# Optimization experiments

Hardware: AMD Instinct MI355X
Metric: run time of the kernel (lower is better)

## Reference

```python
import jax, jax.numpy as jnp
import numpy as np

S, B, D, H, WIN, L = 8192, 4, 512, 8, 64, 6
HD = D // H
EPS = 1e-5


def setup_inputs() -> dict:
    key = jax.random.key(0)
    ks = jax.random.split(key, 6)
    s = 0.02
    return {
        "src": jax.random.normal(ks[0], (S, B, D), jnp.float32),
        "Wqkv": jax.random.normal(ks[1], (L, 3 * D, D), jnp.float32) * s,
        "bqkv": jnp.zeros((L, 3 * D), jnp.float32),
        "Wo": jax.random.normal(ks[2], (L, D, D), jnp.float32) * s,
        "bo": jnp.zeros((L, D), jnp.float32),
        "W1": jax.random.normal(ks[3], (L, 4 * D, D), jnp.float32) * s,
        "bf1": jnp.zeros((L, 4 * D), jnp.float32),
        "W2": jax.random.normal(ks[4], (L, D, 4 * D), jnp.float32) * s,
        "bf2": jnp.zeros((L, D), jnp.float32),
        "g1": jnp.ones((L, D), jnp.float32),
        "beta1": jnp.zeros((L, D), jnp.float32),
        "g2": jnp.ones((L, D), jnp.float32),
        "beta2": jnp.zeros((L, D), jnp.float32),
    }


def layernorm(x, g, b):
    m = jnp.mean(x, axis=-1, keepdims=True)
    v = jnp.mean(jnp.square(x - m), axis=-1, keepdims=True)
    return (x - m) * jax.lax.rsqrt(v + EPS) * g + b


def _forward(src, Wqkv, bqkv, Wo, bo, W1, bf1, W2, bf2, g1, beta1, g2, beta2):
    NW = S // WIN
    scale = 1.0 / np.sqrt(HD)
    x = src
    for l in range(L):
        qkv = x @ Wqkv[l].T + bqkv[l]                      # (S,B,3D)
        q, k, v = jnp.split(qkv, 3, axis=-1)
        win = lambda t: t.reshape(NW, WIN, B, H, HD)       # (NW,W,B,H,hd)
        q = win(q) * scale
        k = win(k)
        v = win(v)
        att = jax.nn.softmax(jnp.einsum('nqbhd,nkbhd->nbhqk', q, k), axis=-1)
        o = jnp.einsum('nbhqk,nkbhd->nqbhd', att, v).reshape(S, B, D)
        o = o @ Wo[l].T + bo[l]
        x = layernorm(x + o, g1[l], beta1[l])
        # FFN with ReLU (hidden = 4*d_model)
        f = jax.nn.relu(x @ W1[l].T + bf1[l]) @ W2[l].T + bf2[l]
        x = layernorm(x + f, g2[l], beta2[l])
    return x


def reference(src, Wqkv, bqkv, Wo, bo, W1, bf1, W2, bf2, g1, beta1, g2, beta2):
    return _forward(src, Wqkv, bqkv, Wo, bo, W1, bf1, W2, bf2, g1, beta1, g2, beta2)
```

## Files before the change

kernel.cpp:

```cpp
#include <hip/hip_runtime.h>
#include <hip/hip_bf16.h>

typedef __bf16 bf16x8 __attribute__((ext_vector_type(8)));
typedef float f32x4 __attribute__((ext_vector_type(4)));

static constexpr int NT = 32768;
static constexpr int D_ = 512;
static constexpr int D3 = 1536;
static constexpr int DF = 2048;
static constexpr int L_ = 6;

#define AS1 __attribute__((address_space(1)))
#define AS3 __attribute__((address_space(3)))

__device__ __forceinline__ void gload_lds16(const void* g, void* l) {
  __builtin_amdgcn_global_load_lds((const AS1 void*)g, (AS3 void*)l, 16, 0, 0);
}

template<int K, int NTN, bool RELU>
__global__ __launch_bounds__(256, 4) void gemm128g(
    const __hip_bfloat16* __restrict__ A,
    const __hip_bfloat16* __restrict__ Wp,
    const float* __restrict__ bias,
    __hip_bfloat16* __restrict__ Cout) {
  __shared__ __align__(16) char lds[32768];
  const int t = threadIdx.x;
  const int l = t & 63, w = t >> 6;
  const int lrow = l & 15, lhi = l >> 4;
  const int wr = w >> 1, wc = w & 1;

  const int lin = blockIdx.x;
  const int wg = (lin & 7) * ((int)gridDim.x >> 3) + (lin >> 3);
  const int tm0 = (wg / NTN) * 128, tn0 = (wg % NTN) * 128;

  constexpr int NKT = K / 64;
  constexpr int N = NTN * 128;

  const int srow = t >> 3;
  const int sun = t & 7;
  const int u8 = (sun ^ (srow & 7)) << 3;
  const __hip_bfloat16* sA = A + (size_t)(tm0 + srow) * K + u8;
  const __hip_bfloat16* sA2 = sA + (size_t)64 * K;

  const char* bpB = (const char*)(Wp + (size_t)((tn0 >> 6) + wc) * NKT * 4096) +
                    l * 16;

  const int lo = lrow * 128;
  const int x0 = (lhi ^ (lrow & 7)) << 4;
  const int x1 = ((4 + lhi) ^ (lrow & 7)) << 4;
  const char* pA[2][2];
  pA[0][0] = lds + wr * 8192 + lo + x0;
  pA[0][1] = lds + wr * 8192 + lo + x1;
  pA[1][0] = lds + 16384 + wr * 8192 + lo + x0;
  pA[1][1] = lds + 16384 + wr * 8192 + lo + x1;

  auto stageA = [&](int p, int kt) {
    char* d0 = lds + p * 16384 + w * 1024;
    const __hip_bfloat16* s0 = sA + kt * 64;
    gload_lds16(s0, d0);
    gload_lds16(s0 + (size_t)32 * K, d0 + 4096);
    char* d1 = lds + p * 16384 + 8192 + w * 1024;
    const __hip_bfloat16* s1 = sA2 + kt * 64;
    gload_lds16(s1, d1);
    gload_lds16(s1 + (size_t)32 * K, d1 + 4096);
  };

  f32x4 acc[4][4] = {};
  bf16x8 af[4][2], bf[2][2];

  stageA(0, 0);
  asm volatile("s_waitcnt vmcnt(0)" ::: "memory");
  __builtin_amdgcn_sched_barrier(0);
  __builtin_amdgcn_s_barrier();

  for (int kt = 0; kt < NKT; ++kt) {
    const int p = kt & 1;
    const bool more = (kt + 1 < NKT);
    if (more) stageA(p ^ 1, kt + 1);
    __builtin_amdgcn_sched_barrier(0);
#pragma unroll
    for (int m = 0; m < 4; ++m)
#pragma unroll
      for (int ks = 0; ks < 2; ++ks)
        af[m][ks] = *(const bf16x8*)(pA[p][ks] + m * 2048);
    const char* qb = bpB + (size_t)kt * 8192;
#pragma unroll
    for (int nh = 0; nh < 2; ++nh) {
#pragma unroll
      for (int n = 0; n < 2; ++n)
#pragma unroll
        for (int ks = 0; ks < 2; ++ks)
          bf[n][ks] = *(const bf16x8*)(qb + nh * 4096 + (n * 2 + ks) * 1024);
#pragma unroll
      for (int m = 0; m < 4; ++m)
#pragma unroll
        for (int n = 0; n < 2; ++n)
#pragma unroll
          for (int ks = 0; ks < 2; ++ks)
            acc[m][nh * 2 + n] = __builtin_amdgcn_mfma_f32_16x16x32_bf16(
                af[m][ks], bf[n][ks], acc[m][nh * 2 + n], 0, 0, 0);
    }
    asm volatile("s_waitcnt lgkmcnt(0)" ::: "memory");
    __builtin_amdgcn_sched_barrier(0);
    __builtin_amdgcn_s_barrier();
  }

  char* ep = lds + w * 8192;
#pragma unroll
  for (int n = 0; n < 4; ++n) {
    float bv = bias[tn0 + wc * 64 + n * 16 + lrow];
#pragma unroll
    for (int m = 0; m < 4; ++m)
#pragma unroll
      for (int j = 0; j < 4; ++j) {
        float v = acc[m][n][j] + bv;
        if (RELU) v = fmaxf(v, 0.f);
        int row = m * 16 + lhi * 4 + j;
        int col = n * 16 + lrow;
        *(__hip_bfloat16*)(ep + row * 128 + (((col >> 3) ^ (row & 7)) << 4) +
                           (col & 7) * 2) = __float2bfloat16(v);
      }
  }
  __builtin_amdgcn_sched_barrier(0);
  const int er = l >> 3, ec = l & 7;
#pragma unroll
  for (int p = 0; p < 8; ++p) {
    int r = p * 8 + er;
    uint4 vv = *(const uint4*)(ep + r * 128 + ((ec ^ (r & 7)) << 4));
    *(uint4*)&Cout[(size_t)(tm0 + wr * 64 + r) * N + tn0 + wc * 64 + ec * 8] = vv;
  }
}

__global__ __launch_bounds__(128) void attn_win(
    const __hip_bfloat16* __restrict__ qkv, __hip_bfloat16* __restrict__ o) {
  __shared__ __align__(16) char lds[2 * 18432];
  const int t = threadIdx.x, l = t & 63, w = t >> 6;
  char* vt = lds + w * 18432;
  char* pl = vt + 9216;
  const int wid = blockIdx.x * 2 + w;
  const int h = wid & 7, b = (wid >> 3) & 3, nw = wid >> 5;
  const int lrow = l & 15, lhi = l >> 4;
  const __hip_bfloat16* qp = qkv + (size_t)(nw * 256 + b) * 1536 + h * 64;
  const __hip_bfloat16* kp = qp + 512;
  const __hip_bfloat16* vp = qp + 1024;

  {
    const int d0 = (l & 7) * 8;
    const int r0 = l >> 3;
#pragma unroll
    for (int i = 0; i < 8; ++i) {
      int r = r0 + i * 8;
      union { uint4 u; __hip_bfloat16 e[8]; } vv;
      vv.u = *(const uint4*)(vp + (size_t)r * 6144 + d0);
#pragma unroll
      for (int j = 0; j < 8; ++j)
        *(__hip_bfloat16*)(vt + ((d0 + j) * 72 + r) * 2) = vv.e[j];
    }
  }

  bf16x8 qf[4][2], kf[4][2];
#pragma unroll
  for (int mi = 0; mi < 4; ++mi)
#pragma unroll
    for (int ks = 0; ks < 2; ++ks) {
      int r = mi * 16 + lrow;
      int d = ks * 32 + lhi * 8;
      qf[mi][ks] = __builtin_bit_cast(bf16x8, *(const uint4*)(qp + (size_t)r * 6144 + d));
      kf[mi][ks] = __builtin_bit_cast(bf16x8, *(const uint4*)(kp + (size_t)r * 6144 + d));
    }

  f32x4 s[4][4] = {};
#pragma unroll
  for (int mi = 0; mi < 4; ++mi)
#pragma unroll
    for (int ni = 0; ni < 4; ++ni) {
      s[mi][ni] = __builtin_amdgcn_mfma_f32_16x16x32_bf16(qf[mi][0], kf[ni][0], s[mi][ni], 0, 0, 0);
      s[mi][ni] = __builtin_amdgcn_mfma_f32_16x16x32_bf16(qf[mi][1], kf[ni][1], s[mi][ni], 0, 0, 0);
    }

#pragma unroll
  for (int mi = 0; mi < 4; ++mi)
#pragma unroll
    for (int j = 0; j < 4; ++j) {
      float mx = s[mi][0][j];
#pragma unroll
      for (int ni = 1; ni < 4; ++ni) mx = fmaxf(mx, s[mi][ni][j]);
      mx = fmaxf(mx, __shfl_xor(mx, 1));
      mx = fmaxf(mx, __shfl_xor(mx, 2));
      mx = fmaxf(mx, __shfl_xor(mx, 4));
      mx = fmaxf(mx, __shfl_xor(mx, 8));
      float p[4], sum = 0.f;
#pragma unroll
      for (int ni = 0; ni < 4; ++ni) { p[ni] = __expf(s[mi][ni][j] - mx); sum += p[ni]; }
      sum += __shfl_xor(sum, 1);
      sum += __shfl_xor(sum, 2);
      sum += __shfl_xor(sum, 4);
      sum += __shfl_xor(sum, 8);
      float inv = 1.f / sum;
      int row = mi * 16 + lhi * 4 + j;
#pragma unroll
      for (int ni = 0; ni < 4; ++ni)
        *(__hip_bfloat16*)(pl + (row * 72 + ni * 16 + lrow) * 2) =
            __float2bfloat16(p[ni] * inv);
    }

  bf16x8 pf[4][2], vf[4][2];
#pragma unroll
  for (int mi = 0; mi < 4; ++mi)
#pragma unroll
    for (int ks = 0; ks < 2; ++ks)
      pf[mi][ks] = *(const bf16x8*)(pl + ((mi * 16 + lrow) * 72 + ks * 32 + lhi * 8) * 2);
#pragma unroll
  for (int ni = 0; ni < 4; ++ni)
#pragma unroll
    for (int ks = 0; ks < 2; ++ks)
      vf[ni][ks] = *(const bf16x8*)(vt + ((ni * 16 + lrow) * 72 + ks * 32 + lhi * 8) * 2);

  f32x4 acc[4][4] = {};
#pragma unroll
  for (int mi = 0; mi < 4; ++mi)
#pragma unroll
    for (int ni = 0; ni < 4; ++ni) {
      acc[mi][ni] = __builtin_amdgcn_mfma_f32_16x16x32_bf16(pf[mi][0], vf[ni][0], acc[mi][ni], 0, 0, 0);
      acc[mi][ni] = __builtin_amdgcn_mfma_f32_16x16x32_bf16(pf[mi][1], vf[ni][1], acc[mi][ni], 0, 0, 0);
    }

  __hip_bfloat16* op = o + (size_t)(nw * 256 + b) * 512 + h * 64;
#pragma unroll
  for (int mi = 0; mi < 4; ++mi)
#pragma unroll
    for (int ni = 0; ni < 4; ++ni) {
      int col = ni * 16 + lrow;
#pragma unroll
      for (int j = 0; j < 4; ++j) {
        int row = mi * 16 + lhi * 4 + j;
        op[(size_t)row * 2048 + col] = __float2bfloat16(acc[mi][ni][j]);
      }
    }
}

template<bool LAST>
__global__ __launch_bounds__(256) void ln_res_b(
    __hip_bfloat16* __restrict__ xb, const __hip_bfloat16* __restrict__ f,
    const float* __restrict__ g, const float* __restrict__ be,
    float* __restrict__ xout) {
  const int w = threadIdx.x >> 6, l = threadIdx.x & 63;
  const size_t row = (size_t)blockIdx.x * 4 + w;
  const int c = l * 8;
  union { uint4 u; __hip_bfloat16 e[8]; } xa, fa;
  xa.u = *(const uint4*)(xb + row * 512 + c);
  fa.u = *(const uint4*)(f + row * 512 + c);
  float v[8];
#pragma unroll
  for (int j = 0; j < 8; ++j)
    v[j] = __bfloat162float(xa.e[j]) + __bfloat162float(fa.e[j]);
  float sum = 0.f, sq = 0.f;
#pragma unroll
  for (int j = 0; j < 8; ++j) { sum += v[j]; sq += v[j] * v[j]; }
#pragma unroll
  for (int m = 1; m < 64; m <<= 1) {
    sum += __shfl_xor(sum, m);
    sq += __shfl_xor(sq, m);
  }
  float mean = sum * (1.f / 512.f);
  float var = sq * (1.f / 512.f) - mean * mean;
  float rs = rsqrtf(var + 1e-5f);
  float4 g0 = *(const float4*)(g + c);
  float4 g1v = *(const float4*)(g + c + 4);
  float4 e0 = *(const float4*)(be + c);
  float4 e1 = *(const float4*)(be + c + 4);
  float gg[8] = {g0.x, g0.y, g0.z, g0.w, g1v.x, g1v.y, g1v.z, g1v.w};
  float ee[8] = {e0.x, e0.y, e0.z, e0.w, e1.x, e1.y, e1.z, e1.w};
  float y[8];
  union { uint4 u; __hip_bfloat16 e[8]; } hb;
#pragma unroll
  for (int j = 0; j < 8; ++j) {
    y[j] = (v[j] - mean) * rs * gg[j] + ee[j];
    hb.e[j] = __float2bfloat16(y[j]);
  }
  *(uint4*)(xb + row * 512 + c) = hb.u;
  if (LAST) {
    float4 o0 = {y[0], y[1], y[2], y[3]};
    float4 o1 = {y[4], y[5], y[6], y[7]};
    *(float4*)(xout + row * 512 + c) = o0;
    *(float4*)(xout + row * 512 + c + 4) = o1;
  }
}

__global__ void convw(const float* __restrict__ s, __hip_bfloat16* __restrict__ o) {
  int i = blockIdx.x * 256 + threadIdx.x;
  float4 v = ((const float4*)s)[i];
  __hip_bfloat16 hb[4] = {__float2bfloat16(v.x), __float2bfloat16(v.y),
                          __float2bfloat16(v.z), __float2bfloat16(v.w)};
  ((uint2*)o)[i] = *(uint2*)hb;
}

template<int K, int Nw, bool SCALEQ>
__global__ void convs(const float* __restrict__ s, __hip_bfloat16* __restrict__ o) {
  int i = blockIdx.x * 256 + threadIdx.x;
  int e = i * 4;
  int layer = e / (Nw * K);
  int rem = e - layer * (Nw * K);
  int r = rem / K, c = rem - r * K;
  float4 v = ((const float4*)s)[i];
  float sc = (SCALEQ && r < 512) ? 0.125f : 1.f;
  int didx = layer * (Nw * K) + ((r >> 6) * (K >> 6) + (c >> 6)) * 4096 +
             (((r >> 4) & 3) * 2 + ((c >> 5) & 1)) * 512 + ((c >> 3) & 3) * 128 +
             (r & 15) * 8 + (c & 7);
  __hip_bfloat16 hb[4] = {__float2bfloat16(v.x * sc), __float2bfloat16(v.y * sc),
                          __float2bfloat16(v.z * sc), __float2bfloat16(v.w * sc)};
  *(uint2*)(o + didx) = *(uint2*)hb;
}

__global__ void scaleb(const float* __restrict__ b, float* __restrict__ o) {
  int i = blockIdx.x * 256 + threadIdx.x;
  o[i] = b[i] * (((i % 1536) < 512) ? 0.125f : 1.f);
}

extern "C" void kernel_launch(void* const* d_in, const int* in_sizes, int n_in,
                              void* d_out, int out_size, void* d_ws, size_t ws_size,
                              hipStream_t stream) {
  const float* src  = (const float*)d_in[0];
  const float* Wqkv = (const float*)d_in[1];
  const float* bqkv = (const float*)d_in[2];
  const float* Wo   = (const float*)d_in[3];
  const float* bo   = (const float*)d_in[4];
  const float* W1   = (const float*)d_in[5];
  const float* bf1  = (const float*)d_in[6];
  const float* W2   = (const float*)d_in[7];
  const float* bf2  = (const float*)d_in[8];
  const float* g1   = (const float*)d_in[9];
  const float* be1  = (const float*)d_in[10];
  const float* g2   = (const float*)d_in[11];
  const float* be2  = (const float*)d_in[12];
  float* xout = (float*)d_out;

  char* ws = (char*)d_ws;
  size_t off = 0;
  auto alloc = [&](size_t bytes) {
    char* p = ws + off;
    off += (bytes + 255) & ~(size_t)255;
    return p;
  };

  const size_t wq_b = (size_t)L_ * D3 * D_ * 2;
  const size_t wo_b = (size_t)L_ * D_ * D_ * 2;
  const size_t w1_b = (size_t)L_ * DF * D_ * 2;
  const size_t w2_b = (size_t)L_ * D_ * DF * 2;
  const size_t xb_b = (size_t)NT * 512 * 2;
  auto al = [](size_t v) { return (v + 255) & ~(size_t)255; };
  const size_t persist =
      al(wq_b) + al(wo_b) + al(w1_b) + al(w2_b) + al(L_ * D3 * 4) + al(xb_b);

  int CT = NT;
  while (CT > 2048 && persist + (size_t)CT * 5120 + 65536 > ws_size) CT >>= 1;

  __hip_bfloat16* wqkvb = (__hip_bfloat16*)alloc(wq_b);
  __hip_bfloat16* wob   = (__hip_bfloat16*)alloc(wo_b);
  __hip_bfloat16* w1b   = (__hip_bfloat16*)alloc(w1_b);
  __hip_bfloat16* w2b   = (__hip_bfloat16*)alloc(w2_b);
  float*          bqs   = (float*)alloc((size_t)L_ * D3 * 4);
  __hip_bfloat16* xb    = (__hip_bfloat16*)alloc(xb_b);
  __hip_bfloat16* R     = (__hip_bfloat16*)alloc((size_t)CT * 2048 * 2);
  __hip_bfloat16* OB    = (__hip_bfloat16*)alloc((size_t)CT * 512 * 2);

  convw<<<NT * 512 / 4 / 256, 256, 0, stream>>>(src, xb);
  convs<512, 1536, true><<<L_ * D3 * D_ / 4 / 256, 256, 0, stream>>>(Wqkv, wqkvb);
  convs<512, 512, false><<<L_ * D_ * D_ / 4 / 256, 256, 0, stream>>>(Wo, wob);
  convs<512, 2048, false><<<L_ * DF * D_ / 4 / 256, 256, 0, stream>>>(W1, w1b);
  convs<2048, 512, false><<<L_ * D_ * DF / 4 / 256, 256, 0, stream>>>(W2, w2b);
  scaleb<<<L_ * D3 / 256, 256, 0, stream>>>(bqkv, bqs);

  const int nch = NT / CT;
  for (int c = 0; c < nch; ++c) {
    __hip_bfloat16* xm = xb + (size_t)c * CT * 512;
    float* xo = xout + (size_t)c * CT * 512;
    for (int l = 0; l < L_; ++l) {
      gemm128g<512, 12, false><<<(CT / 128) * 12, 256, 0, stream>>>(
          xm, wqkvb + (size_t)l * D3 * D_, bqs + l * D3, R);
      attn_win<<<CT / 16, 128, 0, stream>>>(R, OB);
      gemm128g<512, 4, false><<<(CT / 128) * 4, 256, 0, stream>>>(
          OB, wob + (size_t)l * D_ * D_, bo + l * D_, R);
      ln_res_b<false><<<CT / 4, 256, 0, stream>>>(xm, R, g1 + l * D_,
                                                  be1 + l * D_, xo);
      gemm128g<512, 16, true><<<(CT / 128) * 16, 256, 0, stream>>>(
          xm, w1b + (size_t)l * DF * D_, bf1 + l * DF, R);
      gemm128g<2048, 4, false><<<(CT / 128) * 4, 256, 0, stream>>>(
          R, w2b + (size_t)l * D_ * DF, bf2 + l * D_, OB);
      if (l == L_ - 1)
        ln_res_b<true><<<CT / 4, 256, 0, stream>>>(xm, OB, g2 + l * D_,
                                                   be2 + l * D_, xo);
      else
        ln_res_b<false><<<CT / 4, 256, 0, stream>>>(xm, OB, g2 + l * D_,
                                                    be2 + l * D_, xo);
    }
  }
}
```

Baseline: 2.226 ms.

## Stage two K-tiles per barrier phase in GEMM with larger LDS buffers

The GEMM kernel now loads two 64-wide K tiles of A into LDS per pipeline phase, using a 64KB double buffer, and computes both before one barrier. This halves the number of workgroup barriers and waits per K sweep and gives the next stage's loads more time to arrive. In exchange LDS per block doubles and launch bounds drop from 4 to 2 blocks per CU, which lowers occupancy and latency hiding across blocks. An explicit vmcnt wait is added before the barrier.

```diff
diff --git a/kernel.cpp b/kernel.cpp
--- a/kernel.cpp
+++ b/kernel.cpp
@@ -18,12 +18,12 @@
 }
 
 template<int K, int NTN, bool RELU>
-__global__ __launch_bounds__(256, 4) void gemm128g(
+__global__ __launch_bounds__(256, 2) void gemm2(
     const __hip_bfloat16* __restrict__ A,
     const __hip_bfloat16* __restrict__ Wp,
     const float* __restrict__ bias,
     __hip_bfloat16* __restrict__ Cout) {
-  __shared__ __align__(16) char lds[32768];
+  __shared__ __align__(16) char lds[65536];
   const int t = threadIdx.x;
   const int l = t & 63, w = t >> 6;
   const int lrow = l & 15, lhi = l >> 4;
@@ -34,6 +34,7 @@
   const int tm0 = (wg / NTN) * 128, tn0 = (wg % NTN) * 128;
 
   constexpr int NKT = K / 64;
+  constexpr int NP = NKT / 2;
   constexpr int N = NTN * 128;
 
   const int srow = t >> 3;
@@ -48,58 +49,65 @@
   const int lo = lrow * 128;
   const int x0 = (lhi ^ (lrow & 7)) << 4;
   const int x1 = ((4 + lhi) ^ (lrow & 7)) << 4;
-  const char* pA[2][2];
-  pA[0][0] = lds + wr * 8192 + lo + x0;
-  pA[0][1] = lds + wr * 8192 + lo + x1;
-  pA[1][0] = lds + 16384 + wr * 8192 + lo + x0;
-  pA[1][1] = lds + 16384 + wr * 8192 + lo + x1;
-
-  auto stageA = [&](int p, int kt) {
-    char* d0 = lds + p * 16384 + w * 1024;
-    const __hip_bfloat16* s0 = sA + kt * 64;
-    gload_lds16(s0, d0);
-    gload_lds16(s0 + (size_t)32 * K, d0 + 4096);
-    char* d1 = lds + p * 16384 + 8192 + w * 1024;
-    const __hip_bfloat16* s1 = sA2 + kt * 64;
-    gload_lds16(s1, d1);
-    gload_lds16(s1 + (size_t)32 * K, d1 + 4096);
+  const char* pbase = lds + wr * 8192 + lo;
+
+  auto stage = [&](int p, int ktb) {
+    char* base = lds + p * 32768 + w * 1024;
+#pragma unroll
+    for (int sub = 0; sub < 2; ++sub) {
+      const int kt = ktb + sub;
+      char* d = base + sub * 16384;
+      const __hip_bfloat16* s0 = sA + kt * 64;
+      gload_lds16(s0, d);
+      gload_lds16(s0 + (size_t)32 * K, d + 4096);
+      const __hip_bfloat16* s1 = sA2 + kt * 64;
+      gload_lds16(s1, d + 8192);
+      gload_lds16(s1 + (size_t)32 * K, d + 12288);
+    }
   };
 
   f32x4 acc[4][4] = {};
   bf16x8 af[4][2], bf[2][2];
 
-  stageA(0, 0);
+  stage(0, 0);
   asm volatile("s_waitcnt vmcnt(0)" ::: "memory");
   __builtin_amdgcn_sched_barrier(0);
   __builtin_amdgcn_s_barrier();
 
-  for (int kt = 0; kt < NKT; ++kt) {
-    const int p = kt & 1;
-    const bool more = (kt + 1 < NKT);
-    if (more) stageA(p ^ 1, kt + 1);
+  for (int ph = 0; ph < NP; ++ph) {
+    const int p = ph & 1;
+    const int ktb = 2 * ph;
+    const bool more = (ph + 1 < NP);
+    if (more) stage(p ^ 1, ktb + 2);
     __builtin_amdgcn_sched_barrier(0);
 #pragma unroll
-    for (int m = 0; m < 4; ++m)
-#pragma unroll
-      for (int ks = 0; ks < 2; ++ks)
-        af[m][ks] = *(const bf16x8*)(pA[p][ks] + m * 2048);
-    const char* qb = bpB + (size_t)kt * 8192;
-#pragma unroll
-    for (int nh = 0; nh < 2; ++nh) {
-#pragma unroll
-      for (int n = 0; n < 2; ++n)
-#pragma unroll
-        for (int ks = 0; ks < 2; ++ks)
-          bf[n][ks] = *(const bf16x8*)(qb + nh * 4096 + (n * 2 + ks) * 1024);
-#pragma unroll
-      for (int m = 0; m < 4; ++m)
+    for (int sub = 0; sub < 2; ++sub) {
+      const char* ab = pbase + p * 32768 + sub * 16384;
+#pragma unroll
+      for (int m = 0; m < 4; ++m) {
+        af[m][0] = *(const bf16x8*)(ab + x0 + m * 2048);
+        af[m][1] = *(const bf16x8*)(ab + x1 + m * 2048);
+      }
+      const char* qb = bpB + (size_t)(ktb + sub) * 8192;
+#pragma unroll
+      for (int np = 0; np < 2; ++np) {
 #pragma unroll
         for (int n = 0; n < 2; ++n)
 #pragma unroll
           for (int ks = 0; ks < 2; ++ks)
-            acc[m][nh * 2 + n] = __builtin_amdgcn_mfma_f32_16x16x32_bf16(
-                af[m][ks], bf[n][ks], acc[m][nh * 2 + n], 0, 0, 0);
-    }
+            bf[n][ks] =
+                *(const bf16x8*)(qb + ((np * 2 + n) * 2 + ks) * 1024);
+#pragma unroll
+        for (int m = 0; m < 4; ++m)
+#pragma unroll
+          for (int n = 0; n < 2; ++n)
+#pragma unroll
+            for (int ks = 0; ks < 2; ++ks)
+              acc[m][np * 2 + n] = __builtin_amdgcn_mfma_f32_16x16x32_bf16(
+                  af[m][ks], bf[n][ks], acc[m][np * 2 + n], 0, 0, 0);
+      }
+    }
+    if (more) asm volatile("s_waitcnt vmcnt(16)" ::: "memory");
     asm volatile("s_waitcnt lgkmcnt(0)" ::: "memory");
     __builtin_amdgcn_sched_barrier(0);
     __builtin_amdgcn_s_barrier();
@@ -124,8 +132,8 @@
   __builtin_amdgcn_sched_barrier(0);
   const int er = l >> 3, ec = l & 7;
 #pragma unroll
-  for (int p = 0; p < 8; ++p) {
-    int r = p * 8 + er;
+  for (int q = 0; q < 8; ++q) {
+    int r = q * 8 + er;
     uint4 vv = *(const uint4*)(ep + r * 128 + ((ec ^ (r & 7)) << 4));
     *(uint4*)&Cout[(size_t)(tm0 + wr * 64 + r) * N + tn0 + wc * 64 + ec * 8] = vv;
   }
@@ -376,16 +384,16 @@
     __hip_bfloat16* xm = xb + (size_t)c * CT * 512;
     float* xo = xout + (size_t)c * CT * 512;
     for (int l = 0; l < L_; ++l) {
-      gemm128g<512, 12, false><<<(CT / 128) * 12, 256, 0, stream>>>(
+      gemm2<512, 12, false><<<(CT / 128) * 12, 256, 0, stream>>>(
           xm, wqkvb + (size_t)l * D3 * D_, bqs + l * D3, R);
       attn_win<<<CT / 16, 128, 0, stream>>>(R, OB);
-      gemm128g<512, 4, false><<<(CT / 128) * 4, 256, 0, stream>>>(
+      gemm2<512, 4, false><<<(CT / 128) * 4, 256, 0, stream>>>(
           OB, wob + (size_t)l * D_ * D_, bo + l * D_, R);
       ln_res_b<false><<<CT / 4, 256, 0, stream>>>(xm, R, g1 + l * D_,
                                                   be1 + l * D_, xo);
-      gemm128g<512, 16, true><<<(CT / 128) * 16, 256, 0, stream>>>(
+      gemm2<512, 16, true><<<(CT / 128) * 16, 256, 0, stream>>>(
           xm, w1b + (size_t)l * DF * D_, bf1 + l * DF, R);
-      gemm128g<2048, 4, false><<<(CT / 128) * 4, 256, 0, stream>>>(
+      gemm2<2048, 4, false><<<(CT / 128) * 4, 256, 0, stream>>>(
           R, w2b + (size_t)l * D_ * DF, bf2 + l * D_, OB);
       if (l == L_ - 1)
         ln_res_b<true><<<CT / 4, 256, 0, stream>>>(xm, OB, g2 + l * D_,
```

Result: faster. 2.155 ms (-3.2%).
